# Performance work log

Hardware: AMD Instinct MI355X
Metric: run time of the kernel (lower is better)

Reference implementation:

```python
import jax, jax.numpy as jnp
import numpy as np

HIDDEN = 4096


def setup_inputs() -> dict:
    key = jax.random.key(0)
    k1, k2 = jax.random.split(key)
    hidden_states = jax.random.normal(k1, (8, 2048, HIDDEN), dtype=jnp.float32)
    # gate_proj ~ N(0, 0.02^2), shape (2*hidden, hidden)
    gate_proj = 0.02 * jax.random.normal(k2, (2 * HIDDEN, HIDDEN), dtype=jnp.float32)
    return {"hidden_states": hidden_states, "gate_proj": gate_proj, "world_size": 8}


def reference(hidden_states, gate_proj, world_size):
    h = gate_proj.shape[1]
    view = hidden_states.reshape(-1, h)                 # [N, h]
    mm = jnp.einsum("nh,oh->no", view, gate_proj)      # [N, 2h]  (x @ W.T)
    n, o = mm.shape
    # reduce-scatter over dim 0 with world_size ranks: sum the per-rank chunks
    out = mm.reshape(world_size, n // world_size, o).sum(axis=0)  # [N/W, 2h]
    return out
```

## Files before the change

### kernel.cpp

```cpp
#include <hip/hip_runtime.h>
#include <hip/hip_bf16.h>


#define HID   4096
#define SEQ   2048
#define WORLD 8
#define OUTD  8192

typedef __bf16 bf16x8 __attribute__((ext_vector_type(8)));
typedef short  s16x8  __attribute__((ext_vector_type(8)));
typedef float  f32x4  __attribute__((ext_vector_type(4)));

typedef const __attribute__((address_space(1))) void* gas1_ptr;
typedef __attribute__((address_space(3))) void*       las3_ptr;

static __device__ __forceinline__ unsigned short f2bf(float f) {
    union { float f; unsigned u; } v; v.f = f;
    unsigned u = v.u;
    u += 0x7fffu + ((u >> 16) & 1u);
    return (unsigned short)(u >> 16);
}

#define RED_BLOCKS  2048
#define CONV_BLOCKS 4096
__global__ void prep_kernel(const float* __restrict__ hs,
                            const float* __restrict__ w,
                            unsigned short* __restrict__ xb,
                            unsigned short* __restrict__ wb) {
    if (blockIdx.x < RED_BLOCKS) {
        const int total4 = SEQ * HID / 4;
        const float4* h4 = (const float4*)hs;
        ushort4* o4 = (ushort4*)xb;
        for (int i = blockIdx.x * blockDim.x + threadIdx.x; i < total4;
             i += RED_BLOCKS * blockDim.x) {
            float4 s = h4[i];
            #pragma unroll
            for (int ww = 1; ww < WORLD; ++ww) {
                float4 t = h4[i + ww * total4];
                s.x += t.x; s.y += t.y; s.z += t.z; s.w += t.w;
            }
            ushort4 o;
            o.x = f2bf(s.x); o.y = f2bf(s.y); o.z = f2bf(s.z); o.w = f2bf(s.w);
            o4[i] = o;
        }
    } else {
        const int total4 = OUTD * HID / 4;
        const float4* w4 = (const float4*)w;
        ushort4* o4 = (ushort4*)wb;
        for (int i = (blockIdx.x - RED_BLOCKS) * blockDim.x + threadIdx.x;
             i < total4; i += CONV_BLOCKS * blockDim.x) {
            float4 s = w4[i];
            ushort4 o;
            o.x = f2bf(s.x); o.y = f2bf(s.y); o.z = f2bf(s.z); o.w = f2bf(s.w);
            o4[i] = o;
        }
    }
}


#define BM 256
#define BN 256
#define BK 64
#define KSTEPS (HID / BK)

__global__ __launch_bounds__(512, 2)
void gemm_bt_kernel(const unsigned short* __restrict__ A,
                    const unsigned short* __restrict__ B,
                    float* __restrict__ C) {
    __shared__ __align__(16) unsigned short lsA[2][BM * BK];
    __shared__ __align__(16) unsigned short lsB[2][BN * BK];

    const int tid  = threadIdx.x;
    const int lane = tid & 63;
    const int wave = tid >> 6;
    const int wm   = wave >> 2;
    const int wn   = wave & 3;

    const int bid   = blockIdx.x;
    const int xcd   = bid & 7;
    const int local = bid >> 3;
    const int bm = (xcd >> 2) * 4 + (local >> 3);
    const int bn = (xcd & 3) * 8 + (local & 7);

    const int subrow = lane >> 3;
    const int slot   = lane & 7;
    const int scol   = (slot ^ subrow) * 8;
    const unsigned short* aBase =
        A + (size_t)(bm * BM + wave * 8 + subrow) * HID + scol;
    const unsigned short* bBase =
        B + (size_t)(bn * BN + wave * 8 + subrow) * HID + scol;
    const int ldsW = wave * 8 * BK;

#define ST_A(buf, ktv, l) __builtin_amdgcn_global_load_lds(                     \
        (gas1_ptr)(aBase + (size_t)(ktv) * BK + (size_t)(l) * 64 * HID),        \
        (las3_ptr)(&lsA[buf][(l) * 64 * BK + ldsW]), 16, 0, 0)
#define ST_B(buf, ktv, l) __builtin_amdgcn_global_load_lds(                     \
        (gas1_ptr)(bBase + (size_t)(ktv) * BK + (size_t)(l) * 64 * HID),        \
        (las3_ptr)(&lsB[buf][(l) * 64 * BK + ldsW]), 16, 0, 0)
#define STG_A(buf, ktv, h) do { ST_A(buf, ktv, 2*(h)); ST_A(buf, ktv, 2*(h)+1); } while (0)
#define STG_B(buf, ktv, h) do { ST_B(buf, ktv, 2*(h)); ST_B(buf, ktv, 2*(h)+1); } while (0)

    const int fr    = lane & 15;
    const int fq    = lane >> 4;
    const int axor  = fr & 7;
    const int koff0 = ((0 + fq) ^ axor) * 8;
    const int koff1 = ((4 + fq) ^ axor) * 8;
    const int aRowB = (wm * 128 + fr) * BK;
    const int bRowB = (wn * 64 + fr) * BK;

#define RD_A(dst, P, mm, koff) dst = __builtin_bit_cast(bf16x8,                 \
        *(const s16x8*)&lsA[P][aRowB + (mm) * 16 * BK + (koff)])
#define RD_B(dst, P, nn, koff) dst = __builtin_bit_cast(bf16x8,                 \
        *(const s16x8*)&lsB[P][bRowB + (nn) * 16 * BK + (koff)])

#define BARRIER() __builtin_amdgcn_s_barrier()
#define LGKM0()   asm volatile("s_waitcnt lgkmcnt(0)" ::: "memory")
#define VMC6()    asm volatile("s_waitcnt vmcnt(6)" ::: "memory")
#define VMC0()    asm volatile("s_waitcnt vmcnt(0)" ::: "memory")
#define PRIO1()   __builtin_amdgcn_s_setprio(1)
#define PRIO0()   __builtin_amdgcn_s_setprio(0)
#define SB()      __builtin_amdgcn_sched_barrier(0)

#define MFMA16(VAx, mb)                                                          \
    PRIO1();                                                                     \
    _Pragma("unroll")                                                            \
    for (int s = 0; s < 2; ++s)                                                  \
        _Pragma("unroll")                                                        \
        for (int m = 0; m < 2; ++m)                                              \
            _Pragma("unroll")                                                    \
            for (int n = 0; n < 4; ++n)                                          \
                acc[(mb) + m][n] = __builtin_amdgcn_mfma_f32_16x16x32_bf16(      \
                    VAx[m][s], vb[n][s], acc[(mb) + m][n], 0, 0, 0);             \
    PRIO0()

#define TILE_SECTION(P, Q, S, s1, st)                                            \
                                                              \
    BARRIER(); SB();                                                             \
    RD_B(vb[0][0], P, 0, koff0); RD_B(vb[0][1], P, 0, koff1);                    \
    RD_B(vb[1][0], P, 1, koff0); RD_B(vb[1][1], P, 1, koff1);                    \
    RD_B(vb[2][0], P, 2, koff0); RD_B(vb[2][1], P, 2, koff1);                    \
    RD_B(vb[3][0], P, 3, koff0); RD_B(vb[3][1], P, 3, koff1);                    \
    RD_A(va[0][0], P, 0, koff0); RD_A(va[0][1], P, 0, koff1);                    \
    RD_A(va[1][0], P, 1, koff0); RD_A(va[1][1], P, 1, koff1);                    \
    if (s1) STG_A(Q, (S) + 1, 1);                                                \
    LGKM0(); SB();                                                               \
    MFMA16(va, 0);                                                               \
    SB();                                                                        \
                                                              \
    BARRIER(); SB();                                                             \
    RD_A(vc[0][0], P, 2, koff0); RD_A(vc[0][1], P, 2, koff1);                    \
    RD_A(vc[1][0], P, 3, koff0); RD_A(vc[1][1], P, 3, koff1);                    \
    RD_A(va[0][0], P, 4, koff0); RD_A(va[0][1], P, 4, koff1);                    \
    RD_A(va[1][0], P, 5, koff0); RD_A(va[1][1], P, 5, koff1);                    \
    if (st) STG_B(P, (S) + 2, 0);                                                \
    LGKM0(); SB();                                                               \
    MFMA16(vc, 2);                                                               \
    SB();                                                                        \
                                                              \
    BARRIER(); SB();                                                             \
    RD_A(vd[0][0], P, 6, koff0); RD_A(vd[0][1], P, 6, koff1);                    \
    RD_A(vd[1][0], P, 7, koff0); RD_A(vd[1][1], P, 7, koff1);                    \
    if (st) STG_B(P, (S) + 2, 1);                                                \
    LGKM0(); SB();                                                               \
    MFMA16(va, 4);                                                               \
    SB();                                                                        \
                                                              \
    BARRIER(); SB();                                                             \
    if (st) STG_A(P, (S) + 2, 0);                                                \
    MFMA16(vd, 6);                                                               \
    if (st) { VMC6(); } else { VMC0(); }                                         \
    SB()

    f32x4 acc[8][4] = {};
    bf16x8 va[2][2], vc[2][2], vd[2][2], vb[4][2];

    STG_B(0, 0, 0); STG_B(0, 0, 1); STG_A(0, 0, 0); STG_A(0, 0, 1);
    STG_B(1, 1, 0); STG_B(1, 1, 1); STG_A(1, 1, 0);
    VMC6();

    #pragma unroll 1
    for (int t = 0; t < KSTEPS; t += 2) {
        const bool g1 = (t + 1 < KSTEPS), g2 = (t + 2 < KSTEPS), g3 = (t + 3 < KSTEPS);
        TILE_SECTION(0, 1, t,     g1, g2);
        TILE_SECTION(1, 0, t + 1, g2, g3);
    }

    const long crow0 = (long)bm * BM + wm * 128 + fq * 4;
    const long ccol0 = (long)bn * BN + wn * 64 + fr;
    #pragma unroll
    for (int m = 0; m < 8; ++m)
        #pragma unroll
        for (int n = 0; n < 4; ++n)
            #pragma unroll
            for (int j = 0; j < 4; ++j)
                C[(crow0 + m * 16 + j) * OUTD + ccol0 + n * 16] = acc[m][n][j];
}

extern "C" void kernel_launch(void* const* d_in, const int* in_sizes, int n_in,
                              void* d_out, int out_size, void* d_ws, size_t ws_size,
                              hipStream_t stream) {
    const float* hs = (const float*)d_in[0];
    const float* w  = (const float*)d_in[1];
    float* out = (float*)d_out;

    unsigned short* xb = (unsigned short*)d_ws;
    unsigned short* wb = xb + (size_t)SEQ * HID;

    hipLaunchKernelGGL(prep_kernel, dim3(RED_BLOCKS + CONV_BLOCKS), dim3(256),
                       0, stream, hs, w, xb, wb);
    hipLaunchKernelGGL(gemm_bt_kernel, dim3((SEQ / BM) * (OUTD / BN)), dim3(512),
                       0, stream, xb, wb, out);
}
```

Baseline: 220.4 us.

## Switch GEMM inner loop from 16x16x32 to 32x32x16 bf16 MFMA tiles

Replaces the per-wave 128x64 tile computation built from 16x16x32 MFMAs with 32x32x16 MFMAs, reorganizing LDS fragment reads (four k-chunks per 32-row fragment) and accumulator layout and the epilogue store indexing accordingly. The intent is to reduce the LDS read traffic per flop and the MFMA instruction count by using the larger MFMA shape, which reuses each operand fragment across more outputs. It changes register usage and the output write pattern, and the LDS swizzle interaction with 32-lane rows may introduce bank conflicts.

```diff
diff --git a/kernel.cpp b/kernel.cpp
--- a/kernel.cpp
+++ b/kernel.cpp
@@ -7,9 +7,10 @@
 #define WORLD 8
 #define OUTD  8192
 
-typedef __bf16 bf16x8 __attribute__((ext_vector_type(8)));
-typedef short  s16x8  __attribute__((ext_vector_type(8)));
-typedef float  f32x4  __attribute__((ext_vector_type(4)));
+typedef __bf16 bf16x8  __attribute__((ext_vector_type(8)));
+typedef short  s16x8   __attribute__((ext_vector_type(8)));
+typedef float  f32x16  __attribute__((ext_vector_type(16)));
+typedef float  f32x4   __attribute__((ext_vector_type(4)));
 
 typedef const __attribute__((address_space(1))) void* gas1_ptr;
 typedef __attribute__((address_space(3))) void*       las3_ptr;
@@ -100,18 +101,23 @@
 #define STG_A(buf, ktv, h) do { ST_A(buf, ktv, 2*(h)); ST_A(buf, ktv, 2*(h)+1); } while (0)
 #define STG_B(buf, ktv, h) do { ST_B(buf, ktv, 2*(h)); ST_B(buf, ktv, 2*(h)+1); } while (0)
 
-    const int fr    = lane & 15;
-    const int fq    = lane >> 4;
-    const int axor  = fr & 7;
-    const int koff0 = ((0 + fq) ^ axor) * 8;
-    const int koff1 = ((4 + fq) ^ axor) * 8;
-    const int aRowB = (wm * 128 + fr) * BK;
-    const int bRowB = (wn * 64 + fr) * BK;
+    const int fr32  = lane & 31;
+    const int fq2   = lane >> 5;
+    const int axor  = fr32 & 7;
+    const int k0 = ((0 + fq2) ^ axor) * 8;
+    const int k1 = ((2 + fq2) ^ axor) * 8;
+    const int k2 = ((4 + fq2) ^ axor) * 8;
+    const int k3 = ((6 + fq2) ^ axor) * 8;
+    const int aRowB = (wm * 128 + fr32) * BK;
+    const int bRowB = (wn * 64 + fr32) * BK;
 
 #define RD_A(dst, P, mm, koff) dst = __builtin_bit_cast(bf16x8,                 \
-        *(const s16x8*)&lsA[P][aRowB + (mm) * 16 * BK + (koff)])
+        *(const s16x8*)&lsA[P][aRowB + (mm) * 32 * BK + (koff)])
 #define RD_B(dst, P, nn, koff) dst = __builtin_bit_cast(bf16x8,                 \
-        *(const s16x8*)&lsB[P][bRowB + (nn) * 16 * BK + (koff)])
+        *(const s16x8*)&lsB[P][bRowB + (nn) * 32 * BK + (koff)])
+
+#define RD_A4(ARR, P, mm) do { RD_A(ARR[0], P, mm, k0); RD_A(ARR[1], P, mm, k1); \
+                               RD_A(ARR[2], P, mm, k2); RD_A(ARR[3], P, mm, k3); } while (0)
 
 #define BARRIER() __builtin_amdgcn_s_barrier()
 #define LGKM0()   asm volatile("s_waitcnt lgkmcnt(0)" ::: "memory")
@@ -121,58 +127,52 @@
 #define PRIO0()   __builtin_amdgcn_s_setprio(0)
 #define SB()      __builtin_amdgcn_sched_barrier(0)
 
-#define MFMA16(VAx, mb)                                                          \
+#define MFMA32(VAx, mi)                                                          \
     PRIO1();                                                                     \
     _Pragma("unroll")                                                            \
-    for (int s = 0; s < 2; ++s)                                                  \
+    for (int s = 0; s < 4; ++s)                                                  \
         _Pragma("unroll")                                                        \
-        for (int m = 0; m < 2; ++m)                                              \
-            _Pragma("unroll")                                                    \
-            for (int n = 0; n < 4; ++n)                                          \
-                acc[(mb) + m][n] = __builtin_amdgcn_mfma_f32_16x16x32_bf16(      \
-                    VAx[m][s], vb[n][s], acc[(mb) + m][n], 0, 0, 0);             \
+        for (int n = 0; n < 2; ++n)                                              \
+            acc[mi][n] = __builtin_amdgcn_mfma_f32_32x32x16_bf16(                \
+                VAx[s], vb[n][s], acc[mi][n], 0, 0, 0);                          \
     PRIO0()
 
 #define TILE_SECTION(P, Q, S, s1, st)                                            \
-                                                              \
-    BARRIER(); SB();                                                             \
-    RD_B(vb[0][0], P, 0, koff0); RD_B(vb[0][1], P, 0, koff1);                    \
-    RD_B(vb[1][0], P, 1, koff0); RD_B(vb[1][1], P, 1, koff1);                    \
-    RD_B(vb[2][0], P, 2, koff0); RD_B(vb[2][1], P, 2, koff1);                    \
-    RD_B(vb[3][0], P, 3, koff0); RD_B(vb[3][1], P, 3, koff1);                    \
-    RD_A(va[0][0], P, 0, koff0); RD_A(va[0][1], P, 0, koff1);                    \
-    RD_A(va[1][0], P, 1, koff0); RD_A(va[1][1], P, 1, koff1);                    \
+                                        \
+    BARRIER(); SB();                                                             \
+    RD_B(vb[0][0], P, 0, k0); RD_B(vb[0][1], P, 0, k1);                          \
+    RD_B(vb[0][2], P, 0, k2); RD_B(vb[0][3], P, 0, k3);                          \
+    RD_B(vb[1][0], P, 1, k0); RD_B(vb[1][1], P, 1, k1);                          \
+    RD_B(vb[1][2], P, 1, k2); RD_B(vb[1][3], P, 1, k3);                          \
+    RD_A4(va, P, 0);                                                             \
     if (s1) STG_A(Q, (S) + 1, 1);                                                \
     LGKM0(); SB();                                                               \
-    MFMA16(va, 0);                                                               \
+    MFMA32(va, 0);                                                               \
     SB();                                                                        \
-                                                              \
-    BARRIER(); SB();                                                             \
-    RD_A(vc[0][0], P, 2, koff0); RD_A(vc[0][1], P, 2, koff1);                    \
-    RD_A(vc[1][0], P, 3, koff0); RD_A(vc[1][1], P, 3, koff1);                    \
-    RD_A(va[0][0], P, 4, koff0); RD_A(va[0][1], P, 4, koff1);                    \
-    RD_A(va[1][0], P, 5, koff0); RD_A(va[1][1], P, 5, koff1);                    \
+                                                    \
+    BARRIER(); SB();                                                             \
+    RD_A4(vc, P, 1);                                                             \
     if (st) STG_B(P, (S) + 2, 0);                                                \
     LGKM0(); SB();                                                               \
-    MFMA16(vc, 2);                                                               \
+    MFMA32(vc, 1);                                                               \
     SB();                                                                        \
-                                                              \
-    BARRIER(); SB();                                                             \
-    RD_A(vd[0][0], P, 6, koff0); RD_A(vd[0][1], P, 6, koff1);                    \
-    RD_A(vd[1][0], P, 7, koff0); RD_A(vd[1][1], P, 7, koff1);                    \
+                                               \
+    BARRIER(); SB();                                                             \
+    RD_A4(va, P, 2);                                                             \
+    RD_A4(vd, P, 3);                                                             \
     if (st) STG_B(P, (S) + 2, 1);                                                \
     LGKM0(); SB();                                                               \
-    MFMA16(va, 4);                                                               \
+    MFMA32(va, 2);                                                               \
     SB();                                                                        \
-                                                              \
+                                            \
     BARRIER(); SB();                                                             \
     if (st) STG_A(P, (S) + 2, 0);                                                \
-    MFMA16(vd, 6);                                                               \
+    MFMA32(vd, 3);                                                               \
     if (st) { VMC6(); } else { VMC0(); }                                         \
     SB()
 
-    f32x4 acc[8][4] = {};
-    bf16x8 va[2][2], vc[2][2], vd[2][2], vb[4][2];
+    f32x16 acc[4][2] = {};
+    bf16x8 va[4], vc[4], vd[4], vb[2][4];
 
     STG_B(0, 0, 0); STG_B(0, 0, 1); STG_A(0, 0, 0); STG_A(0, 0, 1);
     STG_B(1, 1, 0); STG_B(1, 1, 1); STG_A(1, 1, 0);
@@ -185,15 +185,16 @@
         TILE_SECTION(1, 0, t + 1, g2, g3);
     }
 
-    const long crow0 = (long)bm * BM + wm * 128 + fq * 4;
-    const long ccol0 = (long)bn * BN + wn * 64 + fr;
+    const long crow0 = (long)bm * BM + wm * 128 + fq2 * 4;
+    const long ccol0 = (long)bn * BN + wn * 64 + fr32;
     #pragma unroll
-    for (int m = 0; m < 8; ++m)
+    for (int mi = 0; mi < 4; ++mi)
         #pragma unroll
-        for (int n = 0; n < 4; ++n)
+        for (int n = 0; n < 2; ++n)
             #pragma unroll
-            for (int j = 0; j < 4; ++j)
-                C[(crow0 + m * 16 + j) * OUTD + ccol0 + n * 16] = acc[m][n][j];
+            for (int r = 0; r < 16; ++r)
+                C[(crow0 + mi * 32 + (r & 3) + 8 * (r >> 2)) * OUTD
+                  + ccol0 + n * 32] = acc[mi][n][r];
 }
 
 extern "C" void kernel_launch(void* const* d_in, const int* in_sizes, int n_in,
```

Result: slower. 231.8 us (+5.2%).
